# Optimization experiments

Hardware: AMD Instinct MI355X
Metric: run time of the kernel (lower is better)

Reference implementation:

```python
import jax, jax.numpy as jnp
import numpy as np

B, N, D, K, SD, HD = 32, 4096, 256, 8, 64, 128
NUM_ITERS = 3
EPS = 1e-8
LN_EPS = 1e-5
SCALE = SD ** -0.5


def layer_norm(x, g, b):
    m = jnp.mean(x, axis=-1, keepdims=True)
    v = jnp.mean((x - m) ** 2, axis=-1, keepdims=True)
    return (x - m) * jax.lax.rsqrt(v + LN_EPS) * g + b


def setup_inputs() -> dict:
    key = jax.random.key(0)
    ks = jax.random.split(key, 16)

    def lin(k, out_d, in_d):
        return jax.random.normal(k, (out_d, in_d), jnp.float32) / np.sqrt(in_d).astype(np.float32)

    return {
        "inputs": jax.random.normal(ks[0], (B, N, D), jnp.float32),
        "slot_noise": jax.random.normal(ks[1], (B, K, SD), jnp.float32),
        "slots_mu": jax.random.normal(ks[2], (1, 1, SD), jnp.float32) * 0.1,
        "slots_log_sigma": jnp.zeros((1, 1, SD), jnp.float32),
        "ln_proj_g": jnp.ones((D,), jnp.float32), "ln_proj_b": jnp.zeros((D,), jnp.float32),
        "W_proj": lin(ks[3], SD, D), "b_proj": jnp.zeros((SD,), jnp.float32),
        "Wq": lin(ks[4], SD, SD), "Wk": lin(ks[5], SD, SD), "Wv": lin(ks[6], SD, SD),
        "W_ih": lin(ks[7], 3 * SD, SD), "W_hh": lin(ks[8], 3 * SD, SD),
        "b_ih": jnp.zeros((3 * SD,), jnp.float32), "b_hh": jnp.zeros((3 * SD,), jnp.float32),
        "W_mlp1": lin(ks[9], HD, SD), "b_mlp1": jnp.zeros((HD,), jnp.float32),
        "W_mlp2": lin(ks[10], SD, HD), "b_mlp2": jnp.zeros((SD,), jnp.float32),
        "ln_in_g": jnp.ones((SD,), jnp.float32), "ln_in_b": jnp.zeros((SD,), jnp.float32),
        "ln_slots_g": jnp.ones((SD,), jnp.float32), "ln_slots_b": jnp.zeros((SD,), jnp.float32),
        "ln_mlp_g": jnp.ones((SD,), jnp.float32), "ln_mlp_b": jnp.zeros((SD,), jnp.float32),
    }


def reference(inputs, slot_noise, slots_mu, slots_log_sigma, ln_proj_g, ln_proj_b,
              W_proj, b_proj, Wq, Wk, Wv, W_ih, W_hh, b_ih, b_hh,
              W_mlp1, b_mlp1, W_mlp2, b_mlp2,
              ln_in_g, ln_in_b, ln_slots_g, ln_slots_b, ln_mlp_g, ln_mlp_b):
    # project_input: LayerNorm(D) -> Linear(D, SD)
    x = layer_norm(inputs, ln_proj_g, ln_proj_b) @ W_proj.T + b_proj  # [B,N,SD]
    # init slots from learnable gaussian with externally supplied noise
    slots = slots_mu + jnp.exp(slots_log_sigma) * slot_noise  # [B,K,SD]
    xn = layer_norm(x, ln_in_g, ln_in_b)
    k = xn @ Wk.T  # [B,N,SD]
    v = xn @ Wv.T  # [B,N,SD]

    for _ in range(NUM_ITERS):
        slots_prev = slots
        sn = layer_norm(slots, ln_slots_g, ln_slots_b)
        q = sn @ Wq.T  # [B,K,SD]
        logits = jnp.einsum('bkd,bnd->bkn', q, k) * SCALE
        attn = jax.nn.softmax(logits, axis=1)  # softmax over slots
        w = attn / (jnp.sum(attn, axis=-1, keepdims=True) + EPS)
        updates = jnp.einsum('bkn,bnd->bkd', w, v)  # [B,K,SD]
        # GRUCell(updates, slots_prev)
        gi = updates @ W_ih.T + b_ih  # [B,K,3*SD]
        gh = slots_prev @ W_hh.T + b_hh
        i_r, i_z, i_n = jnp.split(gi, 3, axis=-1)
        h_r, h_z, h_n = jnp.split(gh, 3, axis=-1)
        r = jax.nn.sigmoid(i_r + h_r)
        z = jax.nn.sigmoid(i_z + h_z)
        n = jnp.tanh(i_n + r * h_n)
        slots = (1.0 - z) * n + z * slots_prev
        # residual MLP
        h = jax.nn.relu(layer_norm(slots, ln_mlp_g, ln_mlp_b) @ W_mlp1.T + b_mlp1)
        slots = slots + h @ W_mlp2.T + b_mlp2

    sn = layer_norm(slots, ln_slots_g, ln_slots_b)
    q = sn @ Wq.T
    logits = jnp.einsum('bkd,bnd->bkn', q, k) * SCALE
    final_attn = jax.nn.softmax(logits, axis=1)
    return slots, final_attn
```

## Files before the change

kernel.cpp:

```cpp
#include <hip/hip_runtime.h>

typedef unsigned short u16;
typedef unsigned int   u32;
typedef __attribute__((ext_vector_type(8)))  short short8;
typedef __attribute__((ext_vector_type(4)))  float f32x4v;

#define DEVI __device__ __forceinline__

constexpr int   Bb = 32, Nn = 4096, Dd = 256, Kk = 8, SDd = 64, HDd = 128;
constexpr float EPSc = 1e-8f, LNEPS = 1e-5f, SCALEc = 0.125f;

DEVI u16 f2b(float f) {
  u32 u = __builtin_bit_cast(u32, f);
  return (u16)((u + 0x7fffu + ((u >> 16) & 1u)) >> 16);
}
DEVI float b2f(u16 s) { return __builtin_bit_cast(float, ((u32)s) << 16); }
DEVI float sigmoidf_(float x) { return 1.f / (1.f + __expf(-x)); }

DEVI void gll16(const void* g, void* l) {
  __builtin_amdgcn_global_load_lds(
      (const __attribute__((address_space(1))) u32*)g,
      (__attribute__((address_space(3))) u32*)l, 16, 0, 0);
}

DEVI float dot64(const float* __restrict__ a, const float* __restrict__ w) {
  float s = 0.f;
  #pragma unroll
  for (int i = 0; i < 16; ++i) {
    float4 av = *(const float4*)(a + i * 4);
    float4 wv = *(const float4*)(w + i * 4);
    s += av.x * wv.x + av.y * wv.y + av.z * wv.z + av.w * wv.w;
  }
  return s;
}
DEVI float dotL64(const float* __restrict__ x, const u16* __restrict__ wl, int j) {
  float s = 0.f;
  #pragma unroll
  for (int i = 0; i < 8; ++i) {
    short8 wv8 = *(const short8*)((const char*)wl + ((j * 128 + 16 * i) ^ ((j & 7) << 4)));
    #pragma unroll
    for (int e = 0; e < 8; ++e) s += x[i * 8 + e] * b2f((u16)wv8[e]);
  }
  return s;
}
DEVI float dotL128(const float* __restrict__ x, const u16* __restrict__ wl, int j) {
  float s = 0.f;
  #pragma unroll
  for (int i = 0; i < 16; ++i) {
    short8 wv8 = *(const short8*)((const char*)wl + ((j * 256 + 16 * i) ^ ((j & 7) << 4)));
    #pragma unroll
    for (int e = 0; e < 8; ++e) s += x[i * 8 + e] * b2f((u16)wv8[e]);
  }
  return s;
}

DEVI void ln8(const float* src, float* dst, const float* __restrict__ g,
              const float* __restrict__ b, int t) {
  int l = t & 63, w = t >> 6;
  int r = w * 2 + (l >> 5), c = l & 31;
  float x0 = src[r * 64 + c], x1 = src[r * 64 + c + 32];
  float s = x0 + x1, q2 = x0 * x0 + x1 * x1;
  #pragma unroll
  for (int m = 1; m < 32; m <<= 1) { s += __shfl_xor(s, m); q2 += __shfl_xor(q2, m); }
  float mean = s * (1.f / 64.f);
  float rs = rsqrtf(q2 * (1.f / 64.f) - mean * mean + LNEPS);
  dst[r * 64 + c]      = (x0 - mean) * rs * g[c]      + b[c];
  dst[r * 64 + c + 32] = (x1 - mean) * rs * g[c + 32] + b[c + 32];
}

__global__ __launch_bounds__(256) void k_prep(
    const float* __restrict__ Wp, const float* __restrict__ Wk,
    const float* __restrict__ Wv, const float* __restrict__ W_ih,
    const float* __restrict__ W_hh, const float* __restrict__ W1,
    const float* __restrict__ W2, const float* __restrict__ Wq,
    u16* __restrict__ wp_sw, u16* __restrict__ wk_sw, u16* __restrict__ wv_sw,
    u16* __restrict__ wupd_sw) {
  const int t = threadIdx.x;
  int i = blockIdx.x * 256 + t;
  if (i < 16384) {
    wp_sw[i ^ (((i >> 8) & 7) << 3)] = f2b(Wp[i]);
  } else if (i < 20480) {
    int j = i - 16384; wk_sw[j ^ (((j >> 6) & 7) << 3)] = f2b(Wk[j]);
  } else if (i < 24576) {
    int j = i - 20480; wv_sw[j ^ (((j >> 6) & 7) << 3)] = f2b(Wv[j]);
  } else if (i < 36864) {
    int j = i - 24576; wupd_sw[j ^ (((j >> 6) & 7) << 3)] = f2b(W_ih[j]);
  } else if (i < 49152) {
    int j = i - 36864; wupd_sw[12288 + (j ^ (((j >> 6) & 7) << 3))] = f2b(W_hh[j]);
  } else if (i < 57344) {
    int j = i - 49152; wupd_sw[24576 + (j ^ (((j >> 6) & 7) << 3))] = f2b(W1[j]);
  } else if (i < 65536) {
    int j = i - 57344; wupd_sw[32768 + (j ^ (((j >> 7) & 7) << 3))] = f2b(W2[j]);
  } else if (i < 69632) {
    int j = i - 65536; wupd_sw[40960 + (j ^ (((j >> 6) & 7) << 3))] = f2b(Wq[j]);
  }
}

__global__ __launch_bounds__(512) void k_proj_kv(
    const float* __restrict__ in, const float* __restrict__ gpro,
    const float* __restrict__ bpro, const u16* __restrict__ wp_sw,
    const float* __restrict__ bproj, const float* __restrict__ gin,
    const float* __restrict__ bin, const u16* __restrict__ wk_sw,
    const u16* __restrict__ wv_sw, u16* __restrict__ k_ws,
    u16* __restrict__ v_ws, const u16* __restrict__ wupd_sw,
    const float* __restrict__ noise, const float* __restrict__ mu,
    const float* __restrict__ ls, const float* __restrict__ gs,
    const float* __restrict__ bs, float* __restrict__ q_ws) {
  __shared__ __align__(16) u16 wp_lds[64 * 256];
  __shared__ __align__(16) u16 wk_lds[64 * 64];
  __shared__ __align__(16) u16 wv_lds[64 * 64];
  __shared__ __align__(16) u16 xn_lds[128 * 64];
  __shared__ float gp_l[256], bp_l[256], bj_l[64], gn_l[64], bn_l[64];

  const int t = threadIdx.x;
  const int l = t & 63, w = t >> 6;

  if (blockIdx.x >= 1024) {
    const int b = (int)blockIdx.x - 1024;
    gll16((const char*)wupd_sw + 81920 + t * 16, (char*)wk_lds + t * 16);
    const int d = t & 63, row = t >> 6;
    float x = mu[d] + __expf(ls[d]) * noise[b * 512 + t];
    float s = x, q2 = x * x;
    #pragma unroll
    for (int m = 1; m < 64; m <<= 1) { s += __shfl_xor(s, m); q2 += __shfl_xor(q2, m); }
    float mean = s * (1.f / 64.f);
    float rs = rsqrtf(q2 * (1.f / 64.f) - mean * mean + LNEPS);
    float* snl = (float*)xn_lds;
    snl[t] = (x - mean) * rs * gs[d] + bs[d];
    __syncthreads();
    q_ws[b * 512 + t] = SCALEc * dotL64(snl + row * 64, wk_lds, d);
    return;
  }

  {
    #pragma unroll
    for (int i = 0; i < 4; ++i) {
      int off = w * 4096 + i * 1024 + l * 16;
      gll16((const char*)wp_sw + off, (char*)wp_lds + off);
    }
    {
      int off = w * 1024 + l * 16;
      gll16((const char*)wk_sw + off, (char*)wk_lds + off);
      gll16((const char*)wv_sw + off, (char*)wv_lds + off);
    }
  }
  if (t < 256) { gp_l[t] = gpro[t]; bp_l[t] = bpro[t]; }
  if (t < 64) { bj_l[t] = bproj[t]; gn_l[t] = gin[t]; bn_l[t] = bin[t]; }

  const int r16 = l & 15, q4 = l >> 4;
  const long rowbase = (long)blockIdx.x * 128 + w * 16;
  const long grow = rowbase + r16;
  const float* rp = in + grow * 256;

  short8 a[8];
  float sum = 0.f, sq = 0.f;
  #pragma unroll
  for (int ks = 0; ks < 8; ++ks) {
    float4 L0 = *(const float4*)(rp + ks * 32 + q4 * 8);
    float4 L1 = *(const float4*)(rp + ks * 32 + q4 * 8 + 4);
    sum += L0.x + L0.y + L0.z + L0.w + L1.x + L1.y + L1.z + L1.w;
    sq += L0.x * L0.x + L0.y * L0.y + L0.z * L0.z + L0.w * L0.w +
          L1.x * L1.x + L1.y * L1.y + L1.z * L1.z + L1.w * L1.w;
    a[ks][0] = (short)f2b(L0.x); a[ks][1] = (short)f2b(L0.y);
    a[ks][2] = (short)f2b(L0.z); a[ks][3] = (short)f2b(L0.w);
    a[ks][4] = (short)f2b(L1.x); a[ks][5] = (short)f2b(L1.y);
    a[ks][6] = (short)f2b(L1.z); a[ks][7] = (short)f2b(L1.w);
  }
  __syncthreads();

  sum += __shfl_xor(sum, 16); sum += __shfl_xor(sum, 32);
  sq  += __shfl_xor(sq, 16);  sq  += __shfl_xor(sq, 32);
  float mean = sum * (1.f / 256.f);
  float rs = rsqrtf(sq * (1.f / 256.f) - mean * mean + LNEPS);
  #pragma unroll
  for (int ks = 0; ks < 8; ++ks) {
    #pragma unroll
    for (int j = 0; j < 8; ++j) {
      int kidx = ks * 32 + q4 * 8 + j;
      float x = b2f((u16)a[ks][j]);
      a[ks][j] = (short)f2b((x - mean) * rs * gp_l[kidx] + bp_l[kidx]);
    }
  }

  f32x4v acc[4];
  #pragma unroll
  for (int nt = 0; nt < 4; ++nt)
    #pragma unroll
    for (int i = 0; i < 4; ++i) acc[nt][i] = 0.f;
  #pragma unroll
  for (int ks = 0; ks < 8; ++ks) {
    #pragma unroll
    for (int nt = 0; nt < 4; ++nt) {
      int n = nt * 16 + r16;
      int byte = (n * 512 + 64 * ks + 16 * q4) ^ ((n & 7) << 4);
      short8 bf = *(const short8*)((const char*)wp_lds + byte);
      acc[nt] = __builtin_amdgcn_mfma_f32_16x16x32_bf16(a[ks], bf, acc[nt], 0, 0, 0);
    }
  }
  #pragma unroll
  for (int nt = 0; nt < 4; ++nt) {
    float bb = bj_l[nt * 16 + r16];
    #pragma unroll
    for (int reg = 0; reg < 4; ++reg) acc[nt][reg] += bb;
  }
  #pragma unroll
  for (int reg = 0; reg < 4; ++reg) {
    float s = acc[0][reg] + acc[1][reg] + acc[2][reg] + acc[3][reg];
    float q2 = acc[0][reg] * acc[0][reg] + acc[1][reg] * acc[1][reg] +
               acc[2][reg] * acc[2][reg] + acc[3][reg] * acc[3][reg];
    #pragma unroll
    for (int m = 1; m < 16; m <<= 1) { s += __shfl_xor(s, m); q2 += __shfl_xor(q2, m); }
    float mn = s * (1.f / 64.f);
    float rr = rsqrtf(q2 * (1.f / 64.f) - mn * mn + LNEPS);
    int row = q4 * 4 + reg;
    int rowg = w * 16 + row;
    #pragma unroll
    for (int nt = 0; nt < 4; ++nt) {
      int col = nt * 16 + r16;
      float y = (acc[nt][reg] - mn) * rr * gn_l[col] + bn_l[col];
      int byte = (rowg * 128 + 2 * col) ^ ((row & 7) << 4);
      *(u16*)((char*)xn_lds + byte) = f2b(y);
    }
  }
  __syncthreads();

  f32x4v kacc[4], vacc[4];
  #pragma unroll
  for (int nt = 0; nt < 4; ++nt)
    #pragma unroll
    for (int i = 0; i < 4; ++i) { kacc[nt][i] = 0.f; vacc[nt][i] = 0.f; }
  #pragma unroll
  for (int ks = 0; ks < 2; ++ks) {
    int rowg2 = w * 16 + r16;
    int abyte = (rowg2 * 128 + 64 * ks + 16 * q4) ^ ((r16 & 7) << 4);
    short8 af = *(const short8*)((const char*)xn_lds + abyte);
    #pragma unroll
    for (int nt = 0; nt < 4; ++nt) {
      int n = nt * 16 + r16;
      int bbyte = (n * 128 + 64 * ks + 16 * q4) ^ ((n & 7) << 4);
      short8 bk = *(const short8*)((const char*)wk_lds + bbyte);
      short8 bv = *(const short8*)((const char*)wv_lds + bbyte);
      kacc[nt] = __builtin_amdgcn_mfma_f32_16x16x32_bf16(af, bk, kacc[nt], 0, 0, 0);
      vacc[nt] = __builtin_amdgcn_mfma_f32_16x16x32_bf16(af, bv, vacc[nt], 0, 0, 0);
    }
  }
  #pragma unroll
  for (int nt = 0; nt < 4; ++nt) {
    #pragma unroll
    for (int reg = 0; reg < 4; ++reg) {
      int row = w * 16 + q4 * 4 + reg;
      int col = nt * 16 + r16;
      int idx = (row * 64 + col) ^ ((row & 7) << 3);
      xn_lds[idx] = f2b(kacc[nt][reg]);
    }
  }
  __syncthreads();
  {
    const uint4* src = (const uint4*)xn_lds;
    uint4* dst = (uint4*)(k_ws + (long)blockIdx.x * 8192);
    dst[t] = src[t];
    dst[t + 512] = src[t + 512];
  }
  __syncthreads();
  #pragma unroll
  for (int nt = 0; nt < 4; ++nt) {
    #pragma unroll
    for (int reg = 0; reg < 4; ++reg) {
      int row = w * 16 + q4 * 4 + reg;
      int col = nt * 16 + r16;
      xn_lds[row * 64 + col] = f2b(vacc[nt][reg]);
    }
  }
  __syncthreads();
  {
    const uint4* src = (const uint4*)xn_lds;
    uint4* dst = (uint4*)(v_ws + (long)blockIdx.x * 8192);
    dst[t] = src[t];
    dst[t + 512] = src[t + 512];
  }
}

__global__ __launch_bounds__(128) void k_attn(
    const float* __restrict__ q_ws, const u16* __restrict__ k_img,
    const u16* __restrict__ v_ws, float* __restrict__ S_part,
    float* __restrict__ U_part) {
  const int bx = blockIdx.x, by = blockIdx.y, t = threadIdx.x;
  const int l = t & 63, w = t >> 6;
  __shared__ __align__(16) u16 k_l[8192];
  __shared__ __align__(16) u16 v_l[8192];
  __shared__ float ql[512];
  __shared__ __align__(16) float attn_l[1024];
  __shared__ float sred[16];

  {
    const char* ksrc = (const char*)(k_img + ((long)(by * 32 + bx)) * 8192);
    const char* vsrc = (const char*)(v_ws + ((long)(by * 32 + bx)) * 8192);
    #pragma unroll
    for (int i = 0; i < 8; ++i) {
      int off = i * 2048 + t * 16;
      gll16(ksrc + off, (char*)k_l + off);
      gll16(vsrc + off, (char*)v_l + off);
    }
  }
  for (int i = t; i < 512; i += 128) ql[i] = q_ws[by * 512 + i];
  __syncthreads();

  short8 kw8[8];
  #pragma unroll
  for (int j = 0; j < 8; ++j)
    kw8[j] = *(const short8*)((const char*)k_l + ((t * 128 + 16 * j) ^ ((t & 7) << 4)));
  float lg[8];
  #pragma unroll
  for (int i = 0; i < 8; ++i) lg[i] = 0.f;
  #pragma unroll
  for (int c4 = 0; c4 < 16; ++c4) {
    int j = c4 >> 1, e0 = (c4 & 1) * 4;
    float f0 = b2f((u16)kw8[j][e0]);
    float f1 = b2f((u16)kw8[j][e0 + 1]);
    float f2v = b2f((u16)kw8[j][e0 + 2]);
    float f3 = b2f((u16)kw8[j][e0 + 3]);
    #pragma unroll
    for (int kk = 0; kk < 8; ++kk) {
      float4 qv = *(const float4*)(ql + kk * 64 + c4 * 4);
      lg[kk] += qv.x * f0 + qv.y * f1 + qv.z * f2v + qv.w * f3;
    }
  }
  float mx = lg[0];
  #pragma unroll
  for (int kk = 1; kk < 8; ++kk) mx = fmaxf(mx, lg[kk]);
  float e[8], ss = 0.f;
  #pragma unroll
  for (int kk = 0; kk < 8; ++kk) { e[kk] = __expf(lg[kk] - mx); ss += e[kk]; }
  float inv = 1.f / ss;
  #pragma unroll
  for (int kk = 0; kk < 8; ++kk) e[kk] *= inv;
  float4 A0 = {e[0], e[1], e[2], e[3]}, A1 = {e[4], e[5], e[6], e[7]};
  *(float4*)(attn_l + t * 8) = A0;
  *(float4*)(attn_l + t * 8 + 4) = A1;
  __syncthreads();

  float au[8][2];
  #pragma unroll
  for (int i = 0; i < 8; ++i) { au[i][0] = 0.f; au[i][1] = 0.f; }
  const int p = l & 31, g = l >> 5;
  const u32* vl32 = (const u32*)v_l;
  #pragma unroll 8
  for (int nn = 0; nn < 32; ++nn) {
    int n = nn * 2 + g;
    float4 a0 = *(const float4*)(attn_l + (w * 64 + n) * 8);
    float4 a1 = *(const float4*)(attn_l + (w * 64 + n) * 8 + 4);
    u32 vv = vl32[(w * 64 + n) * 32 + p];
    float vlo = b2f((u16)(vv & 0xffff)), vhi = b2f((u16)(vv >> 16));
    au[0][0] += a0.x * vlo; au[0][1] += a0.x * vhi;
    au[1][0] += a0.y * vlo; au[1][1] += a0.y * vhi;
    au[2][0] += a0.z * vlo; au[2][1] += a0.z * vhi;
    au[3][0] += a0.w * vlo; au[3][1] += a0.w * vhi;
    au[4][0] += a1.x * vlo; au[4][1] += a1.x * vhi;
    au[5][0] += a1.y * vlo; au[5][1] += a1.y * vhi;
    au[6][0] += a1.z * vlo; au[6][1] += a1.z * vhi;
    au[7][0] += a1.w * vlo; au[7][1] += a1.w * vhi;
  }
  #pragma unroll
  for (int kk = 0; kk < 8; ++kk) {
    au[kk][0] += __shfl_xor(au[kk][0], 32);
    au[kk][1] += __shfl_xor(au[kk][1], 32);
  }
  float s8[8];
  #pragma unroll
  for (int kk = 0; kk < 8; ++kk) {
    s8[kk] = e[kk];
    #pragma unroll
    for (int m = 1; m < 64; m <<= 1) s8[kk] += __shfl_xor(s8[kk], m);
  }
  __syncthreads();
  float* ured = attn_l;
  if (l < 32) {
    #pragma unroll
    for (int kk = 0; kk < 8; ++kk) {
      ured[w * 512 + kk * 64 + 2 * p]     = au[kk][0];
      ured[w * 512 + kk * 64 + 2 * p + 1] = au[kk][1];
    }
  }
  if (l == 0) {
    #pragma unroll
    for (int kk = 0; kk < 8; ++kk) sred[w * 8 + kk] = s8[kk];
  }
  __syncthreads();
  for (int i = t; i < 512; i += 128)
    U_part[((long)(by * 32 + bx)) * 512 + i] = ured[i] + ured[512 + i];
  if (t < 8)
    S_part[(by * 32 + bx) * 8 + t] = sred[t] + sred[8 + t];
}

__global__ __launch_bounds__(256) void k_update(
    const float* __restrict__ S_part, const float* __restrict__ U_part,
    const float* __restrict__ slots_in, int init_slots,
    const float* __restrict__ noise, const float* __restrict__ mu,
    const float* __restrict__ ls, const u16* __restrict__ wupd_sw,
    const float* __restrict__ b_ih, const float* __restrict__ b_hh,
    const float* __restrict__ gm, const float* __restrict__ bm,
    const float* __restrict__ b1, const float* __restrict__ b2,
    const float* __restrict__ gs, const float* __restrict__ bs,
    float* __restrict__ slots_out, float* __restrict__ q_ws,
    float* __restrict__ out_slots, int write_out) {
  const int b = blockIdx.x, t = threadIdx.x;
  __shared__ __align__(16) u16 wupd[45056];
  __shared__ float u_l[512], sp[512], gi[1536], gh[1536], sn2[512], mi[512],
      h1[1024], Ssum[8];
  const u16* wih_l = wupd;
  const u16* whh_l = wupd + 12288;
  const u16* w1_l  = wupd + 24576;
  const u16* w2_l  = wupd + 32768;
  const u16* wq_l  = wupd + 40960;

  {
    #pragma unroll
    for (int c = 0; c < 22; ++c) {
      int off = c * 4096 + t * 16;
      gll16((const char*)wupd_sw + off, (char*)wupd + off);
    }
  }
  if (t < 8) {
    float s = 0.f;
    #pragma unroll
    for (int ch = 0; ch < 32; ++ch) s += S_part[(b * 32 + ch) * 8 + t];
    Ssum[t] = s;
  }
  for (int i = t; i < 512; i += 256) {
    float v;
    if (init_slots) { int d = i & 63; v = mu[d] + __expf(ls[d]) * noise[b * 512 + i]; }
    else v = slots_in[b * 512 + i];
    sp[i] = v;
  }
  __syncthreads();
  for (int i = t; i < 512; i += 256) {
    float s = 0.f;
    #pragma unroll
    for (int ch = 0; ch < 32; ++ch) s += U_part[((long)(b * 32 + ch)) * 512 + i];
    u_l[i] = s / (Ssum[i >> 6] + EPSc);
  }
  __syncthreads();
  for (int i = t; i < 1536; i += 256) {
    int kk = i / 192, j = i - kk * 192;
    gi[i] = b_ih[j] + dotL64(u_l + kk * 64, wih_l, j);
    gh[i] = b_hh[j] + dotL64(sp + kk * 64, whh_l, j);
  }
  __syncthreads();
  for (int i = t; i < 512; i += 256) {
    int kk = i >> 6, d = i & 63, base = kk * 192;
    float r = sigmoidf_(gi[base + d] + gh[base + d]);
    float z = sigmoidf_(gi[base + 64 + d] + gh[base + 64 + d]);
    float nn = tanhf(gi[base + 128 + d] + r * gh[base + 128 + d]);
    sn2[i] = (1.f - z) * nn + z * sp[i];
  }
  __syncthreads();
  ln8(sn2, mi, gm, bm, t);
  __syncthreads();
  for (int i = t; i < 1024; i += 256) {
    int kk = i >> 7, j = i & 127;
    h1[i] = fmaxf(b1[j] + dotL64(mi + kk * 64, w1_l, j), 0.f);
  }
  __syncthreads();
  for (int i = t; i < 512; i += 256) {
    int kk = i >> 6, d = i & 63;
    float s = sn2[i] + b2[d] + dotL128(h1 + kk * 128, w2_l, d);
    slots_out[b * 512 + i] = s;
    if (write_out) out_slots[b * 512 + i] = s;
    u_l[i] = s;
  }
  __syncthreads();
  ln8(u_l, mi, gs, bs, t);
  __syncthreads();
  for (int i = t; i < 512; i += 256)
    q_ws[b * 512 + i] = SCALEc * dotL64(mi + (i >> 6) * 64, wq_l, i & 63);
}

__global__ __launch_bounds__(128) void k_final(
    const float* __restrict__ q_ws, const u16* __restrict__ k_img,
    float* __restrict__ outA) {
  const int bx = blockIdx.x, by = blockIdx.y, t = threadIdx.x;
  __shared__ __align__(16) u16 k_l[8192];
  __shared__ float ql[512];
  {
    const char* gsrc = (const char*)(k_img + ((long)(by * 32 + bx)) * 8192);
    #pragma unroll
    for (int i = 0; i < 8; ++i) {
      int off = i * 2048 + t * 16;
      gll16(gsrc + off, (char*)k_l + off);
    }
  }
  for (int i = t; i < 512; i += 128) ql[i] = q_ws[by * 512 + i];
  __syncthreads();
  short8 kw8[8];
  #pragma unroll
  for (int j = 0; j < 8; ++j)
    kw8[j] = *(const short8*)((const char*)k_l + ((t * 128 + 16 * j) ^ ((t & 7) << 4)));
  float lg[8];
  #pragma unroll
  for (int i = 0; i < 8; ++i) lg[i] = 0.f;
  #pragma unroll
  for (int c4 = 0; c4 < 16; ++c4) {
    int j = c4 >> 1, e0 = (c4 & 1) * 4;
    float f0 = b2f((u16)kw8[j][e0]);
    float f1 = b2f((u16)kw8[j][e0 + 1]);
    float f2v = b2f((u16)kw8[j][e0 + 2]);
    float f3 = b2f((u16)kw8[j][e0 + 3]);
    #pragma unroll
    for (int kk = 0; kk < 8; ++kk) {
      float4 qv = *(const float4*)(ql + kk * 64 + c4 * 4);
      lg[kk] += qv.x * f0 + qv.y * f1 + qv.z * f2v + qv.w * f3;
    }
  }
  float mx = lg[0];
  #pragma unroll
  for (int kk = 1; kk < 8; ++kk) mx = fmaxf(mx, lg[kk]);
  float e[8], ss = 0.f;
  #pragma unroll
  for (int kk = 0; kk < 8; ++kk) { e[kk] = __expf(lg[kk] - mx); ss += e[kk]; }
  float inv = 1.f / ss;
  int n = bx * 128 + t;
  #pragma unroll
  for (int kk = 0; kk < 8; ++kk)
    outA[((long)by * 8 + kk) * 4096 + n] = e[kk] * inv;
}

extern "C" void kernel_launch(void* const* d_in, const int* in_sizes, int n_in,
                              void* d_out, int out_size, void* d_ws, size_t ws_size,
                              hipStream_t stream) {
  (void)in_sizes; (void)n_in; (void)out_size; (void)ws_size;
  const float* in    = (const float*)d_in[0];
  const float* noise = (const float*)d_in[1];
  const float* mu    = (const float*)d_in[2];
  const float* ls    = (const float*)d_in[3];
  const float* gpro  = (const float*)d_in[4];
  const float* bpro  = (const float*)d_in[5];
  const float* Wp    = (const float*)d_in[6];
  const float* bproj = (const float*)d_in[7];
  const float* Wq    = (const float*)d_in[8];
  const float* Wk    = (const float*)d_in[9];
  const float* Wv    = (const float*)d_in[10];
  const float* W_ih  = (const float*)d_in[11];
  const float* W_hh  = (const float*)d_in[12];
  const float* b_ih  = (const float*)d_in[13];
  const float* b_hh  = (const float*)d_in[14];
  const float* W1    = (const float*)d_in[15];
  const float* b1    = (const float*)d_in[16];
  const float* W2    = (const float*)d_in[17];
  const float* b2    = (const float*)d_in[18];
  const float* gin   = (const float*)d_in[19];
  const float* bin   = (const float*)d_in[20];
  const float* gs    = (const float*)d_in[21];
  const float* bs    = (const float*)d_in[22];
  const float* gm    = (const float*)d_in[23];
  const float* bm    = (const float*)d_in[24];

  char* ws = (char*)d_ws;
  u16* k_ws      = (u16*)ws;
  u16* v_ws      = (u16*)(ws + 16777216);
  float* S_part  = (float*)(ws + 33554432);
  float* U_part  = (float*)(ws + 33554432 + 32768);
  float* slots_a = (float*)(ws + 33554432 + 32768 + 2097152);
  float* slots_b = (float*)(ws + 33554432 + 32768 + 2097152 + 65536);
  float* q_ws    = (float*)(ws + 33554432 + 32768 + 2097152 + 131072);
  u16* wp_sw     = (u16*)(ws + 33554432 + 32768 + 2097152 + 131072 + 65536);
  u16* wk_sw     = wp_sw + 16384;
  u16* wv_sw     = wk_sw + 4096;
  u16* wupd_sw   = wv_sw + 4096;
  float* out = (float*)d_out;

  k_prep<<<dim3(272), dim3(256), 0, stream>>>(Wp, Wk, Wv, W_ih, W_hh, W1, W2, Wq,
                                              wp_sw, wk_sw, wv_sw, wupd_sw);
  k_proj_kv<<<dim3(1056), dim3(512), 0, stream>>>(in, gpro, bpro, wp_sw, bproj,
                                                  gin, bin, wk_sw, wv_sw, k_ws, v_ws,
                                                  wupd_sw, noise, mu, ls, gs, bs,
                                                  q_ws);
  dim3 ga(32, 32), ba(128);
  k_attn<<<ga, ba, 0, stream>>>(q_ws, k_ws, v_ws, S_part, U_part);
  k_update<<<dim3(32), dim3(256), 0, stream>>>(S_part, U_part, slots_a, 1, noise,
                                               mu, ls, wupd_sw, b_ih, b_hh, gm, bm,
                                               b1, b2, gs, bs, slots_a, q_ws, out, 0);
  k_attn<<<ga, ba, 0, stream>>>(q_ws, k_ws, v_ws, S_part, U_part);
  k_update<<<dim3(32), dim3(256), 0, stream>>>(S_part, U_part, slots_a, 0, noise,
                                               mu, ls, wupd_sw, b_ih, b_hh, gm, bm,
                                               b1, b2, gs, bs, slots_b, q_ws, out, 0);
  k_attn<<<ga, ba, 0, stream>>>(q_ws, k_ws, v_ws, S_part, U_part);
  k_update<<<dim3(32), dim3(256), 0, stream>>>(S_part, U_part, slots_b, 0, noise,
                                               mu, ls, wupd_sw, b_ih, b_hh, gm, bm,
                                               b1, b2, gs, bs, slots_a, q_ws, out, 1);
  k_final<<<ga, ba, 0, stream>>>(q_ws, k_ws, out + 16384);
}
```

Measured before the change: 151.9 us.

## Halve projection block size and keep fp32 inputs for packed bf16 conversion

The projection kernel now processes 64 rows per 256-thread block instead of 128 rows per 512 threads, with twice as many blocks, and the slot-init blocks handle two elements per thread. Input rows are kept in fp32 registers until after the LayerNorm statistics, then normalized and packed to bf16 with a v_cvt_pk_bf16_f32 instruction. This removes the double bf16 round trip and the manual rounding code. Each block still loads the full projection weight into LDS, so total weight staging traffic doubles, and register pressure from holding fp32 inputs rises.

```diff
diff --git a/kernel.cpp b/kernel.cpp
--- a/kernel.cpp
+++ b/kernel.cpp
@@ -4,6 +4,7 @@
 typedef unsigned int   u32;
 typedef __attribute__((ext_vector_type(8)))  short short8;
 typedef __attribute__((ext_vector_type(4)))  float f32x4v;
+typedef __attribute__((ext_vector_type(4)))  u32   u32x4;
 
 #define DEVI __device__ __forceinline__
 
@@ -16,6 +17,11 @@
 }
 DEVI float b2f(u16 s) { return __builtin_bit_cast(float, ((u32)s) << 16); }
 DEVI float sigmoidf_(float x) { return 1.f / (1.f + __expf(-x)); }
+DEVI u32 cvtpk(float lo, float hi) {
+  u32 r;
+  asm("v_cvt_pk_bf16_f32 %0, %1, %2" : "=v"(r) : "v"(lo), "v"(hi));
+  return r;
+}
 
 DEVI void gll16(const void* g, void* l) {
   __builtin_amdgcn_global_load_lds(
@@ -96,7 +102,7 @@
   }
 }
 
-__global__ __launch_bounds__(512) void k_proj_kv(
+__global__ __launch_bounds__(256) void k_proj_kv(
     const float* __restrict__ in, const float* __restrict__ gpro,
     const float* __restrict__ bpro, const u16* __restrict__ wp_sw,
     const float* __restrict__ bproj, const float* __restrict__ gin,
@@ -109,62 +115,69 @@
   __shared__ __align__(16) u16 wp_lds[64 * 256];
   __shared__ __align__(16) u16 wk_lds[64 * 64];
   __shared__ __align__(16) u16 wv_lds[64 * 64];
-  __shared__ __align__(16) u16 xn_lds[128 * 64];
+  __shared__ __align__(16) u16 xn_lds[64 * 64];
   __shared__ float gp_l[256], bp_l[256], bj_l[64], gn_l[64], bn_l[64];
 
-  const int t = threadIdx.x;
-  const int l = t & 63, w = t >> 6;
-
-  if (blockIdx.x >= 1024) {
-    const int b = (int)blockIdx.x - 1024;
+  const int t = threadIdx.x, l = t & 63, w = t >> 6;
+
+  if (blockIdx.x >= 2048) {
+    const int b = (int)blockIdx.x - 2048;
     gll16((const char*)wupd_sw + 81920 + t * 16, (char*)wk_lds + t * 16);
-    const int d = t & 63, row = t >> 6;
-    float x = mu[d] + __expf(ls[d]) * noise[b * 512 + t];
-    float s = x, q2 = x * x;
-    #pragma unroll
-    for (int m = 1; m < 64; m <<= 1) { s += __shfl_xor(s, m); q2 += __shfl_xor(q2, m); }
-    float mean = s * (1.f / 64.f);
-    float rs = rsqrtf(q2 * (1.f / 64.f) - mean * mean + LNEPS);
+    gll16((const char*)wupd_sw + 81920 + 4096 + t * 16,
+          (char*)wk_lds + 4096 + t * 16);
     float* snl = (float*)xn_lds;
-    snl[t] = (x - mean) * rs * gs[d] + bs[d];
+    #pragma unroll
+    for (int h = 0; h < 2; ++h) {
+      int idx = h * 256 + t, d = idx & 63;
+      float x = mu[d] + __expf(ls[d]) * noise[b * 512 + idx];
+      float s = x, q2 = x * x;
+      #pragma unroll
+      for (int m = 1; m < 64; m <<= 1) { s += __shfl_xor(s, m); q2 += __shfl_xor(q2, m); }
+      float mean = s * (1.f / 64.f);
+      float rs = rsqrtf(q2 * (1.f / 64.f) - mean * mean + LNEPS);
+      snl[idx] = (x - mean) * rs * gs[d] + bs[d];
+    }
     __syncthreads();
-    q_ws[b * 512 + t] = SCALEc * dotL64(snl + row * 64, wk_lds, d);
+    #pragma unroll
+    for (int h = 0; h < 2; ++h) {
+      int idx = h * 256 + t, d = idx & 63, row = idx >> 6;
+      q_ws[b * 512 + idx] = SCALEc * dotL64(snl + row * 64, wk_lds, d);
+    }
     return;
   }
 
   {
     #pragma unroll
-    for (int i = 0; i < 4; ++i) {
-      int off = w * 4096 + i * 1024 + l * 16;
+    for (int i = 0; i < 8; ++i) {
+      int off = w * 8192 + i * 1024 + l * 16;
       gll16((const char*)wp_sw + off, (char*)wp_lds + off);
     }
-    {
-      int off = w * 1024 + l * 16;
+    #pragma unroll
+    for (int i = 0; i < 2; ++i) {
+      int off = w * 2048 + i * 1024 + l * 16;
       gll16((const char*)wk_sw + off, (char*)wk_lds + off);
       gll16((const char*)wv_sw + off, (char*)wv_lds + off);
     }
   }
-  if (t < 256) { gp_l[t] = gpro[t]; bp_l[t] = bpro[t]; }
+  gp_l[t] = gpro[t];
+  bp_l[t] = bpro[t];
   if (t < 64) { bj_l[t] = bproj[t]; gn_l[t] = gin[t]; bn_l[t] = bin[t]; }
 
   const int r16 = l & 15, q4 = l >> 4;
-  const long rowbase = (long)blockIdx.x * 128 + w * 16;
-  const long grow = rowbase + r16;
-  const float* rp = in + grow * 256;
-
-  short8 a[8];
+  const long rowbase = (long)blockIdx.x * 64 + w * 16;
+  const float* rp = in + (rowbase + r16) * 256;
+
+  float4 x0[8], x1[8];
   float sum = 0.f, sq = 0.f;
   #pragma unroll
   for (int ks = 0; ks < 8; ++ks) {
-    float4 L0 = *(const float4*)(rp + ks * 32 + q4 * 8);
-    float4 L1 = *(const float4*)(rp + ks * 32 + q4 * 8 + 4);
-    sum += L0.x + L0.y + L0.z + L0.w + L1.x + L1.y + L1.z + L1.w;
-    sq += L0.x * L0.x + L0.y * L0.y + L0.z * L0.z + L0.w * L0.w +
-          L1.x * L1.x + L1.y * L1.y + L1.z * L1.z + L1.w * L1.w;
-    a[ks][0] = (short)f2b(L0.x); a[ks][1] = (short)f2b(L0.y);
-    a[ks][2] = (short)f2b(L0.z); a[ks][3] = (short)f2b(L0.w);
-    a[ks][4] = (short)f2b(L1.x); a[ks][5] = (short)f2b(L1.y);
-    a[ks][6] = (short)f2b(L1.z); a[ks][7] = (short)f2b(L1.w);
+    x0[ks] = *(const float4*)(rp + ks * 32 + q4 * 8);
+    x1[ks] = *(const float4*)(rp + ks * 32 + q4 * 8 + 4);
+    sum += x0[ks].x + x0[ks].y + x0[ks].z + x0[ks].w +
+           x1[ks].x + x1[ks].y + x1[ks].z + x1[ks].w;
+    sq += x0[ks].x * x0[ks].x + x0[ks].y * x0[ks].y + x0[ks].z * x0[ks].z +
+          x0[ks].w * x0[ks].w + x1[ks].x * x1[ks].x + x1[ks].y * x1[ks].y +
+          x1[ks].z * x1[ks].z + x1[ks].w * x1[ks].w;
   }
   __syncthreads();
 
@@ -172,14 +185,23 @@
   sq  += __shfl_xor(sq, 16);  sq  += __shfl_xor(sq, 32);
   float mean = sum * (1.f / 256.f);
   float rs = rsqrtf(sq * (1.f / 256.f) - mean * mean + LNEPS);
+
+  short8 a[8];
   #pragma unroll
   for (int ks = 0; ks < 8; ++ks) {
-    #pragma unroll
-    for (int j = 0; j < 8; ++j) {
-      int kidx = ks * 32 + q4 * 8 + j;
-      float x = b2f((u16)a[ks][j]);
-      a[ks][j] = (short)f2b((x - mean) * rs * gp_l[kidx] + bp_l[kidx]);
-    }
+    int kb = ks * 32 + q4 * 8;
+    float n0 = (x0[ks].x - mean) * rs * gp_l[kb + 0] + bp_l[kb + 0];
+    float n1 = (x0[ks].y - mean) * rs * gp_l[kb + 1] + bp_l[kb + 1];
+    float n2 = (x0[ks].z - mean) * rs * gp_l[kb + 2] + bp_l[kb + 2];
+    float n3 = (x0[ks].w - mean) * rs * gp_l[kb + 3] + bp_l[kb + 3];
+    float n4 = (x1[ks].x - mean) * rs * gp_l[kb + 4] + bp_l[kb + 4];
+    float n5 = (x1[ks].y - mean) * rs * gp_l[kb + 5] + bp_l[kb + 5];
+    float n6 = (x1[ks].z - mean) * rs * gp_l[kb + 6] + bp_l[kb + 6];
+    float n7 = (x1[ks].w - mean) * rs * gp_l[kb + 7] + bp_l[kb + 7];
+    u32x4 pv;
+    pv.x = cvtpk(n0, n1); pv.y = cvtpk(n2, n3);
+    pv.z = cvtpk(n4, n5); pv.w = cvtpk(n6, n7);
+    a[ks] = __builtin_bit_cast(short8, pv);
   }
 
   f32x4v acc[4];
@@ -244,6 +266,7 @@
       vacc[nt] = __builtin_amdgcn_mfma_f32_16x16x32_bf16(af, bv, vacc[nt], 0, 0, 0);
     }
   }
+  __syncthreads();
   #pragma unroll
   for (int nt = 0; nt < 4; ++nt) {
     #pragma unroll
@@ -257,9 +280,9 @@
   __syncthreads();
   {
     const uint4* src = (const uint4*)xn_lds;
-    uint4* dst = (uint4*)(k_ws + (long)blockIdx.x * 8192);
+    uint4* dst = (uint4*)(k_ws + (long)blockIdx.x * 4096);
     dst[t] = src[t];
-    dst[t + 512] = src[t + 512];
+    dst[t + 256] = src[t + 256];
   }
   __syncthreads();
   #pragma unroll
@@ -274,9 +297,9 @@
   __syncthreads();
   {
     const uint4* src = (const uint4*)xn_lds;
-    uint4* dst = (uint4*)(v_ws + (long)blockIdx.x * 8192);
+    uint4* dst = (uint4*)(v_ws + (long)blockIdx.x * 4096);
     dst[t] = src[t];
-    dst[t + 512] = src[t + 512];
+    dst[t + 256] = src[t + 256];
   }
 }
 
@@ -570,7 +593,7 @@
 
   k_prep<<<dim3(272), dim3(256), 0, stream>>>(Wp, Wk, Wv, W_ih, W_hh, W1, W2, Wq,
                                               wp_sw, wk_sw, wv_sw, wupd_sw);
-  k_proj_kv<<<dim3(1056), dim3(512), 0, stream>>>(in, gpro, bpro, wp_sw, bproj,
+  k_proj_kv<<<dim3(2080), dim3(256), 0, stream>>>(in, gpro, bpro, wp_sw, bproj,
                                                   gin, bin, wk_sw, wv_sw, k_ws, v_ws,
                                                   wupd_sw, noise, mu, ls, gs, bs,
                                                   q_ws);
```

New measurement: 150.7 us. Within noise of the previous version (-0.8%).
